# Kernel tuning notes

Measured on AMD Instinct MI355X. Metric: run time of the kernel, lower is better.

## Reference

```python
import jax, jax.numpy as jnp
import numpy as np
from jax import lax

K = 3          # dynamic filter kernel size
NH = 8         # attention heads

def _conv2d(x, w, b, pad, groups=1):
    y = lax.conv_general_dilated(x, w, (1, 1), [(pad, pad), (pad, pad)],
                                 feature_group_count=groups,
                                 dimension_numbers=('NCHW', 'OIHW', 'NCHW'))
    return y + b[None, :, None, None]

def _pw(x, w, b):  # 1x1 conv: w (O,C)
    return jnp.einsum('oc,bchw->bohw', w, x) + b[None, :, None, None]

def _lrelu(x):
    return jnp.where(x >= 0, x, 0.2 * x)

def _unfold(x, k):  # (B,C,H,W) -> (B,C,k*k,H,W), matches F.unfold ordering
    p = k // 2
    xp = jnp.pad(x, ((0, 0), (0, 0), (p, p), (p, p)))
    H, W = x.shape[2], x.shape[3]
    return jnp.stack([xp[:, :, i:i + H, j:j + W] for i in range(k) for j in range(k)], axis=2)

def setup_inputs() -> dict:
    key = jax.random.key(0)
    ks = jax.random.split(key, 24)
    B, C, H, W = 1, 256, 56, 56
    C2, K2 = C // 2, K * K
    s = 0.02
    d = {
        'dec_feat': jax.random.normal(ks[0], (B, C, H, W), jnp.float32),
        'enc_feat': jax.random.normal(ks[1], (B, C, H, W), jnp.float32),
        # ALPF kernel predictor: depthwise 3x3, 1x1 C->C/2, 1x1 C/2->k^2
        'alpf_dw_w': jax.random.normal(ks[2], (C, 1, 3, 3), jnp.float32) * s,
        'alpf_dw_b': jnp.zeros((C,), jnp.float32),
        'alpf_p1_w': jax.random.normal(ks[3], (C2, C), jnp.float32) * s,
        'alpf_p1_b': jnp.zeros((C2,), jnp.float32),
        'alpf_p2_w': jax.random.normal(ks[4], (K2, C2), jnp.float32) * s,
        'alpf_p2_b': jnp.zeros((K2,), jnp.float32),
        # AHPF weight predictor: 3x3 C->C/2, 1x1 C/2->k^2
        'ahpf_c1_w': jax.random.normal(ks[5], (C2, C, 3, 3), jnp.float32) * s,
        'ahpf_c1_b': jnp.zeros((C2,), jnp.float32),
        'ahpf_c2_w': jax.random.normal(ks[6], (K2, C2), jnp.float32) * s,
        'ahpf_c2_b': jnp.zeros((K2,), jnp.float32),
        # cross-attention projections (all 1x1)
        'q_w': jax.random.normal(ks[7], (C, C), jnp.float32) * s,
        'q_b': jnp.zeros((C,), jnp.float32),
        'kv_w': jax.random.normal(ks[8], (2 * C, C), jnp.float32) * s,
        'kv_b': jnp.zeros((2 * C,), jnp.float32),
        'out_w': jax.random.normal(ks[9], (C, C), jnp.float32) * s,
        'out_b': jnp.zeros((C,), jnp.float32),
        # fusion 3x3 conv
        'fusion_w': jax.random.normal(ks[10], (C, C, 3, 3), jnp.float32) * s,
        'fusion_b': jnp.zeros((C,), jnp.float32),
    }
    return d

def _forward(dec_feat, enc_feat, alpf_dw_w, alpf_dw_b, alpf_p1_w, alpf_p1_b,
             alpf_p2_w, alpf_p2_b, ahpf_c1_w, ahpf_c1_b, ahpf_c2_w, ahpf_c2_b,
             q_w, q_b, kv_w, kv_b, out_w, out_b, fusion_w, fusion_b):
    B, C, H, W = dec_feat.shape
    K2 = K * K
    # ---- Adaptive low-pass filter on dec_feat ----
    kw = _conv2d(dec_feat, alpf_dw_w, alpf_dw_b, pad=1, groups=C)
    kw = _lrelu(_pw(kw, alpf_p1_w, alpf_p1_b))
    kw = _pw(kw, alpf_p2_w, alpf_p2_b)            # (B,k2,H,W)
    kw = jax.nn.softmax(kw, axis=1)
    patches = _unfold(dec_feat, K)                # (B,C,k2,H,W)
    f_smooth = jnp.sum(patches * kw[:, None], axis=2)
    # ---- Cross attention: q from f_smooth, kv from enc_feat ----
    hd = C // NH
    N = H * W
    q = _pw(f_smooth, q_w, q_b).reshape(B, NH, hd, N)
    kv = _pw(enc_feat, kv_w, kv_b)
    k, v = jnp.split(kv, 2, axis=1)
    k = k.reshape(B, NH, hd, N)
    v = v.reshape(B, NH, hd, N)
    scale = hd ** -0.5
    attn = jnp.einsum('bhdn,bhdm->bhnm', q, k) * scale
    attn = jax.nn.softmax(attn, axis=-1)
    out = jnp.einsum('bhnm,bhdm->bhdn', attn, v).reshape(B, C, H, W)
    f_aligned = _pw(out, out_w, out_b)
    # ---- Adaptive high-pass filter on enc_feat ----
    wlp = _lrelu(_conv2d(enc_feat, ahpf_c1_w, ahpf_c1_b, pad=1))
    wlp = jax.nn.softmax(_pw(wlp, ahpf_c2_w, ahpf_c2_b), axis=1)  # (B,k2,H,W)
    whp = (-wlp).at[:, K2 // 2].add(1.0)          # delta - W_LP
    epatches = _unfold(enc_feat, K)
    f_high = enc_feat + jnp.sum(epatches * whp[:, None], axis=2)
    # ---- Fusion (w = 1.0) ----
    return _conv2d(f_aligned + 1.0 * f_high, fusion_w, fusion_b, pad=1)

def reference(dec_feat, enc_feat, alpf_dw_w, alpf_dw_b, alpf_p1_w, alpf_p1_b,
              alpf_p2_w, alpf_p2_b, ahpf_c1_w, ahpf_c1_b, ahpf_c2_w, ahpf_c2_b,
              q_w, q_b, kv_w, kv_b, out_w, out_b, fusion_w, fusion_b):
    return _forward(dec_feat, enc_feat, alpf_dw_w, alpf_dw_b, alpf_p1_w, alpf_p1_b,
                    alpf_p2_w, alpf_p2_b, ahpf_c1_w, ahpf_c1_b, ahpf_c2_w, ahpf_c2_b,
                    q_w, q_b, kv_w, kv_b, out_w, out_b, fusion_w, fusion_b)
```

## Files before the change

kernel.cpp:

```cpp
#include <hip/hip_runtime.h>
#include <hip/hip_bf16.h>

#define HH  56
#define WWC 56
#define HWP 3136
#define CC  256
#define NSPLIT 6

typedef unsigned short u16;
typedef __attribute__((ext_vector_type(8))) u16 u16x8;
typedef __attribute__((ext_vector_type(4))) u16 u16x4;
typedef __attribute__((ext_vector_type(8))) short s16x8;
typedef __attribute__((ext_vector_type(4))) float f32x4;

__device__ __forceinline__ u16 f2b(float f) {
  unsigned int x = __float_as_uint(f);
  return (u16)((x + 0x7fffu + ((x >> 16) & 1u)) >> 16);
}
__device__ __forceinline__ float b2f(u16 u) {
  return __uint_as_float(((unsigned int)u) << 16);
}
__device__ __forceinline__ f32x4 mfma16(s16x8 a, s16x8 b, f32x4 c) {
  return __builtin_amdgcn_mfma_f32_16x16x32_bf16(a, b, c, 0, 0, 0);
}

__device__ __forceinline__ float ldsel(const void* p, int i, bool bf) {
  if (bf) return __bfloat162float(((const __hip_bfloat16*)p)[i]);
  return ((const float*)p)[i];
}
__device__ __forceinline__ void stsel(void* p, int i, float v, bool bf) {
  if (bf) ((__hip_bfloat16*)p)[i] = __float2bfloat16(v);
  else ((float*)p)[i] = v;
}

__device__ __forceinline__ void ldrow8(const void* p, size_t i, bool bf,
                                       float* o) {
  if (bf) {
    u16x8 v = *(const u16x8*)((const u16*)p + i);
    #pragma unroll
    for (int j = 0; j < 8; ++j) o[j] = b2f(v[j]);
  } else {
    const float* f = (const float*)p + i;
    f32x4 a = *(const f32x4*)f;
    f32x4 b = *(const f32x4*)(f + 4);
    #pragma unroll
    for (int j = 0; j < 4; ++j) { o[j] = a[j]; o[4 + j] = b[j]; }
  }
}

__global__ void detect_dtype_k(const void* x, float* flag) {
  __shared__ int sh[256];
  int tid = threadIdx.x;
  const __hip_bfloat16* xb = (const __hip_bfloat16*)x;
  int ok = 0;
  for (int i = tid; i < 1024; i += 256) {
    float v = fabsf(__bfloat162float(xb[2 * i]));
    if (v > 9.5e-7f && v < 1.05e6f) ok++;
  }
  sh[tid] = ok;
  __syncthreads();
  for (int s = 128; s > 0; s >>= 1) {
    if (tid < s) sh[tid] += sh[tid + s];
    __syncthreads();
  }
  if (tid == 0) flag[0] = (sh[0] > 512) ? 1.f : 0.f;
}

__global__ __launch_bounds__(256)
void pack_all_k(const void* __restrict__ p1, const void* __restrict__ q,
                const void* __restrict__ kv, const void* __restrict__ ow,
                const void* __restrict__ c1, const void* __restrict__ fu,
                u16* __restrict__ d_p1, u16* __restrict__ d_q,
                u16* __restrict__ d_kv, u16* __restrict__ d_ow,
                u16* __restrict__ d_c1, u16* __restrict__ d_fu,
                const float* __restrict__ dflag) {
  bool bf = dflag[0] > 0.5f;
  int b = blockIdx.x, tid = threadIdx.x;
  if (b < 128) { int g = b * 256 + tid; d_p1[g] = f2b(ldsel(p1, g, bf)); return; }
  b -= 128;
  if (b < 256) { int g = b * 256 + tid; d_q[g] = f2b(ldsel(q, g, bf)); return; }
  b -= 256;
  if (b < 512) { int g = b * 256 + tid; d_kv[g] = f2b(ldsel(kv, g, bf)); return; }
  b -= 512;
  if (b < 256) { int g = b * 256 + tid; d_ow[g] = f2b(ldsel(ow, g, bf)); return; }
  b -= 256;
  if (b < 128) {
    int g = b * 256 + tid;
    #pragma unroll
    for (int t = 0; t < 9; ++t)
      d_c1[(size_t)t * 32768 + g] = f2b(ldsel(c1, g * 9 + t, bf));
    return;
  }
  b -= 128;
  {
    int g = b * 256 + tid;
    #pragma unroll
    for (int t = 0; t < 9; ++t)
      d_fu[(size_t)t * 65536 + g] = f2b(ldsel(fu, g * 9 + t, bf));
  }
}

__device__ __forceinline__ void dwconv_body(int gid, const void* x,
                                            const void* wt, const void* bs,
                                            u16* y, bool bf) {
  int c = gid / 392, g = gid - c * 392;
  int p0 = g * 8;
  int h = p0 / WWC, w0 = p0 - h * WWC;
  float wv[9];
  #pragma unroll
  for (int t = 0; t < 9; ++t) wv[t] = ldsel(wt, c * 9 + t, bf);
  float bv = ldsel(bs, c, bf);
  float acc[8];
  #pragma unroll
  for (int j = 0; j < 8; ++j) acc[j] = bv;
  const size_t cbase = (size_t)c * HWP;
  #pragma unroll
  for (int dh = -1; dh <= 1; ++dh) {
    int hh = h + dh;
    if (hh < 0 || hh >= HH) continue;
    size_t rbase = cbase + hh * WWC + w0;
    float v[8];
    ldrow8(x, rbase, bf, v);
    float lft = (w0 > 0) ? ldsel(x, rbase - 1, bf) : 0.f;
    float rgt = (w0 < 48) ? ldsel(x, rbase + 8, bf) : 0.f;
    float wm = wv[(dh + 1) * 3 + 0], wc = wv[(dh + 1) * 3 + 1],
          wp = wv[(dh + 1) * 3 + 2];
    #pragma unroll
    for (int j = 0; j < 8; ++j) {
      float vm = (j == 0) ? lft : v[j - 1];
      float vp = (j == 7) ? rgt : v[j + 1];
      acc[j] += vm * wm + v[j] * wc + vp * wp;
    }
  }
  u16x8 st;
  #pragma unroll
  for (int j = 0; j < 8; ++j) st[j] = f2b(acc[j]);
  *(u16x8*)&y[cbase + p0] = st;
}

template<int TAPS, int ACT, bool ADDIN, int OMODE>
__device__ __forceinline__ void mgemm_body(
    int bid, int sz, int NZ, int NO, int O,
    const u16* __restrict__ Wp, const void* __restrict__ X,
    const void* __restrict__ bias, const u16* __restrict__ addin,
    void* __restrict__ Y, int Cin, bool wbf, bool xbf, int xmode,
    int bias_off, u16 (*Ws)[72], u16 (*Xs)[72]) {
  int p0 = (bid / NO) * 32, o0 = (bid % NO) * 32;
  int t0 = (TAPS * sz) / NZ, t1 = (TAPS * (sz + 1)) / NZ;
  int tid = threadIdx.x, lane = tid & 63, wv = tid >> 6;
  int oq = (wv & 1) * 16, pq = (wv >> 1) * 16;
  int frow = lane & 15, kgrp = (lane >> 4) * 8;
  int wol = tid >> 3, wkk = (tid & 7) * 8;
  int pl = tid & 31, xkk = (tid >> 5) * 8;
  int p = p0 + pl, h = p / WWC, w = p - h * WWC;
  f32x4 acc = {0.f, 0.f, 0.f, 0.f};
  for (int t = t0; t < t1; ++t) {
    int dh = t / 3 - 1, dw = t % 3 - 1;
    int hh = h + dh, ww = w + dw;
    bool rowok = (TAPS == 1) || ((hh >= 0) && (hh < HH) && (ww >= 0) && (ww < WWC));
    int xoff = (TAPS == 1) ? p : hh * WWC + ww;
    const u16* Wrow = Wp + (size_t)t * O * Cin;
    for (int kb = 0; kb < Cin; kb += 64) {
      __syncthreads();
      *(u16x8*)&Ws[wol][wkk] =
          *(const u16x8*)&Wrow[(size_t)(o0 + wol) * Cin + kb + wkk];
      {
        u16x8 xv;
        if (xmode == 2) {
          if (rowok) {
            xv = *(const u16x8*)&((const u16*)X)[(size_t)xoff * Cin + kb + xkk];
          } else {
            #pragma unroll
            for (int j = 0; j < 8; ++j) xv[j] = 0;
          }
        } else if (xmode == 3) {
          #pragma unroll
          for (int j = 0; j < 8; ++j)
            xv[j] = rowok ? ((const u16*)X)[(size_t)(kb + xkk + j) * HWP + xoff]
                          : (u16)0;
        } else {
          #pragma unroll
          for (int j = 0; j < 8; ++j) {
            int kk = xkk + j;
            float v = rowok ? ldsel(X, (size_t)(kb + kk) * HWP + xoff, xbf) : 0.f;
            xv[j] = f2b(v);
          }
        }
        *(u16x8*)&Xs[pl][xkk] = xv;
      }
      __syncthreads();
      #pragma unroll
      for (int ks = 0; ks < 2; ++ks) {
        s16x8 aw = *(const s16x8*)&Ws[oq + frow][ks * 32 + kgrp];
        s16x8 ax = *(const s16x8*)&Xs[pq + frow][ks * 32 + kgrp];
        acc = mfma16(aw, ax, acc);
      }
    }
  }
  int orow = (lane >> 4) * 4;
  int ogb = o0 + oq + orow;
  int pg = p0 + pq + frow;
  if (OMODE == 4) {
    float* Yp = (float*)Y + (size_t)sz * O * HWP;
    #pragma unroll
    for (int r = 0; r < 4; ++r)
      Yp[(size_t)(ogb + r) * HWP + pg] = acc[r];
  } else if (OMODE == 5) {
    if (ogb < 256) {
      u16x4 st;
      #pragma unroll
      for (int r = 0; r < 4; ++r)
        st[r] = f2b(acc[r] + ldsel(bias, ogb + r, wbf));
      *(u16x4*)&((u16*)Y)[(size_t)pg * 256 + ogb] = st;
    } else {
      u16* V = (u16*)Y + (size_t)CC * HWP;
      #pragma unroll
      for (int r = 0; r < 4; ++r)
        V[(size_t)(ogb + r - 256) * HWP + pg] =
            f2b(acc[r] + ldsel(bias, ogb + r, wbf));
    }
  } else if (OMODE == 2) {
    u16x4 st;
    #pragma unroll
    for (int r = 0; r < 4; ++r) {
      float yv = acc[r] + ldsel(bias, bias_off + ogb + r, wbf);
      if (ACT == 1) yv = (yv >= 0.f) ? yv : 0.2f * yv;
      if (ADDIN) yv += b2f(addin[(size_t)(ogb + r) * HWP + pg]);
      st[r] = f2b(yv);
    }
    *(u16x4*)&((u16*)Y)[(size_t)pg * O + ogb] = st;
  } else {
    #pragma unroll
    for (int r = 0; r < 4; ++r) {
      int og = ogb + r;
      float yv = acc[r] + ldsel(bias, bias_off + og, wbf);
      if (ACT == 1) yv = (yv >= 0.f) ? yv : 0.2f * yv;
      if (ADDIN) yv += b2f(addin[(size_t)og * HWP + pg]);
      if (OMODE == 3) ((u16*)Y)[(size_t)og * HWP + pg] = f2b(yv);
      else stsel(Y, (size_t)og * HWP + pg, yv, (OMODE == 1) && wbf);
    }
  }
}

template<int TAPS, int ACT, bool ADDIN, int OMODE>
__global__ __launch_bounds__(256)
void mgemm32_k(const u16* __restrict__ Wp, const void* __restrict__ X,
               const void* __restrict__ bias, const u16* __restrict__ addin,
               void* __restrict__ Y, int Cin,
               const float* __restrict__ dflag, int xmode, int bias_off) {
  __shared__ u16 Ws[32][72];
  __shared__ u16 Xs[32][72];
  bool wbf = dflag[0] > 0.5f;
  bool xbf = (xmode == 1) ? wbf : false;
  int NO = gridDim.y;
  int bid = blockIdx.x + blockIdx.y * gridDim.x;
  mgemm_body<TAPS, ACT, ADDIN, OMODE>(bid, blockIdx.z, gridDim.z, NO, NO * 32,
                                      Wp, X, bias, addin, Y, Cin, wbf, xbf,
                                      xmode, bias_off, Ws, Xs);
}

__global__ __launch_bounds__(256)
void stage1_k(const void* __restrict__ dec, const void* __restrict__ dw_w,
              const void* __restrict__ dw_b, u16* __restrict__ A,
              const u16* __restrict__ wp_kv, const void* __restrict__ enc,
              const void* __restrict__ kv_b, u16* __restrict__ k16,
              const float* __restrict__ dflag) {
  __shared__ u16 Ws[32][72];
  __shared__ u16 Xs[32][72];
  bool bf = dflag[0] > 0.5f;
  int b = blockIdx.x;
  if (b < 392) {
    dwconv_body(b * 256 + threadIdx.x, dec, dw_w, dw_b, A, bf);
  } else {
    mgemm_body<1, 0, false, 5>(b - 392, 0, 1, 16, 512, wp_kv, enc, kv_b,
                               nullptr, k16, 256, bf, bf, 1, 0, Ws, Xs);
  }
}

__global__ __launch_bounds__(256)
void stage2_k(const u16* __restrict__ Op, const float* __restrict__ Lb,
              u16* __restrict__ A, const u16* __restrict__ wp_c1,
              const void* __restrict__ enc, float* __restrict__ Pc1,
              const float* __restrict__ dflag) {
  __shared__ u16 Ws[32][72];
  __shared__ u16 Xs[32][72];
  bool bf = dflag[0] > 0.5f;
  int b = blockIdx.x;
  if (b < 392) {
    int gid = b * 256 + threadIdx.x;
    int hd = gid / 392, g = gid - hd * 392;
    int n0 = g * 8, h = hd >> 5;
    float L[8] = {0,0,0,0,0,0,0,0}, O[8] = {0,0,0,0,0,0,0,0};
    #pragma unroll
    for (int s = 0; s < NSPLIT; ++s) {
      const float* Lp = &Lb[(size_t)(s * 8 + h) * HWP + n0];
      f32x4 l0 = *(const f32x4*)Lp;
      f32x4 l1 = *(const f32x4*)(Lp + 4);
      u16x8 ov = *(const u16x8*)&Op[(size_t)(s * 256 + hd) * HWP + n0];
      #pragma unroll
      for (int j = 0; j < 4; ++j) { L[j] += l0[j]; L[4 + j] += l1[j]; }
      #pragma unroll
      for (int j = 0; j < 8; ++j) O[j] += b2f(ov[j]);
    }
    u16x8 st;
    #pragma unroll
    for (int j = 0; j < 8; ++j) st[j] = f2b(O[j] / L[j]);
    *(u16x8*)&A[(size_t)hd * HWP + n0] = st;
  } else {
    int rem = b - 392;
    int sz = rem / 392, bb = rem - sz * 392;
    mgemm_body<9, 1, false, 4>(bb, sz, 3, 4, 128, wp_c1, enc, nullptr,
                               nullptr, Pc1, 256, bf, bf, 1, 0, Ws, Xs);
  }
}

__global__ __launch_bounds__(256)
void comb3_v2_k(const float* __restrict__ P, const void* __restrict__ bias,
                u16* __restrict__ Y, const float* __restrict__ dflag) {
  bool bf = dflag[0] > 0.5f;
  int flat = (blockIdx.x * 256 + threadIdx.x) * 4;
  int o = flat / HWP;
  f32x4 a = *(const f32x4*)&P[flat];
  f32x4 b = *(const f32x4*)&P[flat + 128 * HWP];
  f32x4 c = *(const f32x4*)&P[flat + 2 * 128 * HWP];
  float bv = ldsel(bias, o, bf);
  u16x4 st;
  #pragma unroll
  for (int j = 0; j < 4; ++j) {
    float v = a[j] + b[j] + c[j] + bv;
    v = (v >= 0.f) ? v : 0.2f * v;
    st[j] = f2b(v);
  }
  *(u16x4*)&Y[flat] = st;
}

__global__ __launch_bounds__(256)
void comb2_v2_k(const float* __restrict__ P, const void* __restrict__ bias,
                void* __restrict__ Y, const float* __restrict__ dflag) {
  bool bf = dflag[0] > 0.5f;
  int flat = (blockIdx.x * 256 + threadIdx.x) * 4;
  int o = flat / HWP;
  f32x4 a = *(const f32x4*)&P[flat];
  f32x4 b = *(const f32x4*)&P[flat + 256 * HWP];
  float bv = ldsel(bias, o, bf);
  if (bf) {
    u16x4 st;
    #pragma unroll
    for (int j = 0; j < 4; ++j) st[j] = f2b(a[j] + b[j] + bv);
    *(u16x4*)&((u16*)Y)[flat] = st;
  } else {
    f32x4 st;
    #pragma unroll
    for (int j = 0; j < 4; ++j) st[j] = a[j] + b[j] + bv;
    *(f32x4*)&((float*)Y)[flat] = st;
  }
}

template<bool DELTA>
__global__ __launch_bounds__(256)
void pw9_v2_k(const void* __restrict__ w2, const void* __restrict__ b2,
              const u16* __restrict__ hid, u16* __restrict__ out9,
              const float* __restrict__ dflag) {
  bool bf = dflag[0] > 0.5f;
  __shared__ float Wl[9][128];
  __shared__ float Pl[4][9][33];
  int tid = threadIdx.x;
  for (int i = tid; i < 1152; i += 256) Wl[i >> 7][i & 127] = ldsel(w2, i, bf);
  __syncthreads();
  int pix = tid & 31, cig = tid >> 5;
  int p = blockIdx.x * 32 + pix;
  int ci0 = cig * 16;
  float acc[9] = {0.f, 0.f, 0.f, 0.f, 0.f, 0.f, 0.f, 0.f, 0.f};
  #pragma unroll
  for (int j = 0; j < 16; ++j) {
    float xv = b2f(hid[(size_t)(ci0 + j) * HWP + p]);
    #pragma unroll
    for (int t = 0; t < 9; ++t) acc[t] += Wl[t][ci0 + j] * xv;
  }
  #pragma unroll
  for (int t = 0; t < 9; ++t) acc[t] += __shfl_xor(acc[t], 32);
  int wv = tid >> 6;
  if ((tid & 63) < 32) {
    #pragma unroll
    for (int t = 0; t < 9; ++t) Pl[wv][t][pix] = acc[t];
  }
  __syncthreads();
  if (tid < 32) {
    float a[9];
    #pragma unroll
    for (int t = 0; t < 9; ++t)
      a[t] = Pl[0][t][pix] + Pl[1][t][pix] + Pl[2][t][pix] + Pl[3][t][pix] +
             ldsel(b2, t, bf);
    float mx = a[0];
    #pragma unroll
    for (int t = 1; t < 9; ++t) mx = fmaxf(mx, a[t]);
    float s = 0.f;
    #pragma unroll
    for (int t = 0; t < 9; ++t) { a[t] = __expf(a[t] - mx); s += a[t]; }
    float inv = 1.f / s;
    #pragma unroll
    for (int t = 0; t < 9; ++t) {
      float v = a[t] * inv;
      if (DELTA) v = ((t == 4) ? 1.f : 0.f) - v;
      out9[(size_t)t * HWP + p] = f2b(v);
    }
  }
}

template<bool HIGH>
__global__ __launch_bounds__(128)
void spatial_v2_k(const void* __restrict__ x, const u16* __restrict__ w9,
                  u16* __restrict__ y, const float* __restrict__ dflag) {
  bool bf = dflag[0] > 0.5f;
  int gid = blockIdx.x * 128 + threadIdx.x;
  int c = gid / 392, g = gid - c * 392;
  int p0 = g * 8;
  int h = p0 / WWC, w0 = p0 - h * WWC;
  const size_t cbase = (size_t)c * HWP;
  float acc[8];
  if (HIGH) {
    ldrow8(x, cbase + p0, bf, acc);
  } else {
    #pragma unroll
    for (int j = 0; j < 8; ++j) acc[j] = 0.f;
  }
  #pragma unroll
  for (int dh = -1; dh <= 1; ++dh) {
    int hh = h + dh;
    if (hh < 0 || hh >= HH) continue;
    size_t rbase = cbase + hh * WWC + w0;
    float v[8];
    ldrow8(x, rbase, bf, v);
    float lft = (w0 > 0) ? ldsel(x, rbase - 1, bf) : 0.f;
    float rgt = (w0 < 48) ? ldsel(x, rbase + 8, bf) : 0.f;
    float wm[8], wc[8], wp[8];
    {
      int tb = (dh + 1) * 3;
      u16x8 a = *(const u16x8*)&w9[(size_t)(tb + 0) * HWP + p0];
      u16x8 b = *(const u16x8*)&w9[(size_t)(tb + 1) * HWP + p0];
      u16x8 d = *(const u16x8*)&w9[(size_t)(tb + 2) * HWP + p0];
      #pragma unroll
      for (int j = 0; j < 8; ++j) { wm[j] = b2f(a[j]); wc[j] = b2f(b[j]); wp[j] = b2f(d[j]); }
    }
    #pragma unroll
    for (int j = 0; j < 8; ++j) {
      float vm = (j == 0) ? lft : v[j - 1];
      float vp = (j == 7) ? rgt : v[j + 1];
      acc[j] += vm * wm[j] + v[j] * wc[j] + vp * wp[j];
    }
  }
  u16x8 st;
  #pragma unroll
  for (int j = 0; j < 8; ++j) st[j] = f2b(acc[j]);
  *(u16x8*)&y[cbase + p0] = st;
}

__global__ __launch_bounds__(256)
void attn_part_k(const u16* __restrict__ Qb, const u16* __restrict__ Kb,
                 const u16* __restrict__ Vb, u16* __restrict__ Op,
                 float* __restrict__ Lb) {
  __shared__ u16 Ks[64][40];
  __shared__ u16 Vs[32][72];
  __shared__ u16 Ps[4][16][72];
  int h = blockIdx.y, n0 = blockIdx.x * 64, sz = blockIdx.z;
  int tid = threadIdx.x, lane = tid & 63, wv = tid >> 6;
  int frow = lane & 15, gq = lane >> 4, kgrp = gq * 8;
  int ml = tid >> 2, dseg = (tid & 3) * 8;
  int vd = tid >> 3, vm = (tid & 7) * 8;
  const float QS = 0.17677669529663687f * 1.4426950408889634f;
  s16x8 aq;
  {
    u16x8 qv = *(const u16x8*)&Qb[(size_t)(n0 + wv * 16 + frow) * 256 + h * 32 + kgrp];
    u16x8 qs;
    #pragma unroll
    for (int j = 0; j < 8; ++j) qs[j] = f2b(b2f(qv[j]) * QS);
    aq = *(s16x8*)&qs;
  }
  f32x4 oa0 = {0.f, 0.f, 0.f, 0.f}, oa1 = {0.f, 0.f, 0.f, 0.f};
  float lsum = 0.f;
  int t_begin = (49 * sz) / NSPLIT, t_end = (49 * (sz + 1)) / NSPLIT;
  u16x8 kreg = *(const u16x8*)&Kb[(size_t)(t_begin * 64 + ml) * 256 + h * 32 + dseg];
  u16x8 vreg = *(const u16x8*)&Vb[(size_t)(h * 32 + vd) * HWP + t_begin * 64 + vm];
  for (int t = t_begin; t < t_end; ++t) {
    __syncthreads();
    *(u16x8*)&Ks[ml][dseg] = kreg;
    *(u16x8*)&Vs[vd][vm] = vreg;
    if (t + 1 < t_end) {
      kreg = *(const u16x8*)&Kb[(size_t)((t + 1) * 64 + ml) * 256 + h * 32 + dseg];
      vreg = *(const u16x8*)&Vb[(size_t)(h * 32 + vd) * HWP + (t + 1) * 64 + vm];
    }
    __syncthreads();
    f32x4 zero = {0.f, 0.f, 0.f, 0.f};
    #pragma unroll
    for (int fm = 0; fm < 4; ++fm) {
      s16x8 ak = *(const s16x8*)&Ks[fm * 16 + frow][kgrp];
      f32x4 s = mfma16(ak, aq, zero);
      u16x4 pe;
      #pragma unroll
      for (int r = 0; r < 4; ++r) {
        float e = exp2f(fminf(s[r], 43.f));
        lsum += e;
        pe[r] = (u16)(__float_as_uint(e) >> 16);
      }
      *(u16x4*)&Ps[wv][frow][fm * 16 + gq * 4] = pe;
    }
    #pragma unroll
    for (int ks = 0; ks < 2; ++ks) {
      s16x8 ap = *(const s16x8*)&Ps[wv][frow][ks * 32 + kgrp];
      s16x8 bv0 = *(const s16x8*)&Vs[frow][ks * 32 + kgrp];
      s16x8 bv1 = *(const s16x8*)&Vs[16 + frow][ks * 32 + kgrp];
      oa0 = mfma16(ap, bv0, oa0);
      oa1 = mfma16(ap, bv1, oa1);
    }
  }
  lsum += __shfl_xor(lsum, 16);
  lsum += __shfl_xor(lsum, 32);
  if (lane < 16)
    Lb[(size_t)(sz * 8 + h) * HWP + n0 + wv * 16 + frow] = lsum;
  #pragma unroll
  for (int r = 0; r < 4; ++r) {
    int n = n0 + wv * 16 + gq * 4 + r;
    Op[(size_t)(sz * 256 + h * 32 + frow) * HWP + n]      = f2b(oa0[r]);
    Op[(size_t)(sz * 256 + h * 32 + 16 + frow) * HWP + n] = f2b(oa1[r]);
  }
}

extern "C" void kernel_launch(void* const* d_in, const int* in_sizes, int n_in,
                              void* d_out, int out_size, void* d_ws, size_t ws_size,
                              hipStream_t stream) {
  const void* dec   = d_in[0];
  const void* enc   = d_in[1];
  const void* dw_w  = d_in[2];
  const void* dw_b  = d_in[3];
  const void* p1_w  = d_in[4];
  const void* p1_b  = d_in[5];
  const void* p2_w  = d_in[6];
  const void* p2_b  = d_in[7];
  const void* c1_w  = d_in[8];
  const void* c1_b  = d_in[9];
  const void* c2_w  = d_in[10];
  const void* c2_b  = d_in[11];
  const void* q_w   = d_in[12];
  const void* q_b   = d_in[13];
  const void* kv_w  = d_in[14];
  const void* kv_b  = d_in[15];
  const void* out_w = d_in[16];
  const void* out_b = d_in[17];
  const void* fu_w  = d_in[18];
  const void* fu_b  = d_in[19];

  const int CH = CC * HWP;
  float* flag = (float*)d_ws;
  u16* pk     = (u16*)(flag + 8);
  u16* A      = pk;              pk += CH;
  u16* hid    = pk;              pk += 128 * HWP;
  u16* s9     = pk;              pk += 9 * HWP;
  u16* Bb     = pk;              pk += CH;
  u16* qb16   = pk;              pk += CH;
  u16* k16    = pk;              pk += CH;
  u16* v16    = pk;              pk += CH;
  u16* wp_p1  = pk;              pk += 128 * 256;
  u16* wp_q   = pk;              pk += 256 * 256;
  u16* wp_kv  = pk;              pk += 512 * 256;
  u16* wp_out = pk;              pk += 256 * 256;
  u16* wp_c1  = pk;              pk += 128 * 256 * 9;
  u16* wp_fu  = pk;              pk += 256 * 256 * 9;
  pk += (size_t)(-(intptr_t)pk) & 7;
  float* Lb   = (float*)pk;
  u16* Opart  = (u16*)(Lb + 48 * HWP);
  float* Pc1 = (float*)qb16;
  float* Pfu = Lb;

  dim3 blk(256);
  detect_dtype_k<<<1, blk, 0, stream>>>(dec, flag);

  pack_all_k<<<1536, blk, 0, stream>>>(p1_w, q_w, kv_w, out_w, c1_w, fu_w,
                                       wp_p1, wp_q, wp_kv, wp_out, wp_c1, wp_fu,
                                       flag);

  stage1_k<<<1960, blk, 0, stream>>>(dec, dw_w, dw_b, A, wp_kv, enc, kv_b,
                                     k16, flag);

  mgemm32_k<1, 1, false, 3><<<dim3(98, 4), blk, 0, stream>>>(
      wp_p1, A, p1_b, nullptr, hid, 256, flag, 3, 0);
  pw9_v2_k<false><<<98, blk, 0, stream>>>(p2_w, p2_b, hid, s9, flag);
  spatial_v2_k<false><<<784, dim3(128), 0, stream>>>(dec, s9, Bb, flag);
  mgemm32_k<1, 0, false, 2><<<dim3(98, 8), blk, 0, stream>>>(
      wp_q, Bb, q_b, nullptr, qb16, 256, flag, 3, 0);

  attn_part_k<<<dim3(49, 8, NSPLIT), blk, 0, stream>>>(qb16, k16, v16, Opart, Lb);

  stage2_k<<<1568, blk, 0, stream>>>(Opart, Lb, A, wp_c1, enc, Pc1, flag);

  comb3_v2_k<<<392, blk, 0, stream>>>(Pc1, c1_b, hid, flag);
  pw9_v2_k<true><<<98, blk, 0, stream>>>(c2_w, c2_b, hid, s9, flag);
  spatial_v2_k<true><<<784, dim3(128), 0, stream>>>(enc, s9, Bb, flag);

  mgemm32_k<1, 0, true, 2><<<dim3(98, 8), blk, 0, stream>>>(
      wp_out, A, out_b, Bb, qb16, 256, flag, 3, 0);

  mgemm32_k<9, 0, false, 4><<<dim3(98, 8, 2), blk, 0, stream>>>(
      wp_fu, qb16, nullptr, nullptr, Pfu, 256, flag, 2, 0);
  comb2_v2_k<<<784, blk, 0, stream>>>(Pfu, fu_b, d_out, flag);
}
```

Before: 146.0 us.

## Rebuild launch schedule to co-run AHPF branch with ALPF stages before attention

Moves the enc_feat high-pass branch (3x3 conv, combine, pw9 softmax, spatial filter) out of the post-attention section and pairs each of its stages with an independent low-pass or q-projection stage in merged kernels. Duplicate buffers (hid2, s9b, Bb2) keep the two branches from overwriting each other. The attention split-combine becomes a standalone kernel. The fusion 3x3 conv now splits its K dimension three ways with a 3-way reduction instead of two. The goal is fewer serial launches and better GPU fill from concurrent independent work, at the cost of more workspace memory and some extra partial-sum traffic.

```diff
diff --git a/kernel.cpp b/kernel.cpp
--- a/kernel.cpp
+++ b/kernel.cpp
@@ -136,6 +136,100 @@
   #pragma unroll
   for (int j = 0; j < 8; ++j) st[j] = f2b(acc[j]);
   *(u16x8*)&y[cbase + p0] = st;
+}
+
+template<bool HIGH>
+__device__ __forceinline__ void spatial_body(int gid, const void* x,
+                                             const u16* w9, u16* y, bool bf) {
+  int c = gid / 392, g = gid - c * 392;
+  int p0 = g * 8;
+  int h = p0 / WWC, w0 = p0 - h * WWC;
+  const size_t cbase = (size_t)c * HWP;
+  float acc[8];
+  if (HIGH) {
+    ldrow8(x, cbase + p0, bf, acc);
+  } else {
+    #pragma unroll
+    for (int j = 0; j < 8; ++j) acc[j] = 0.f;
+  }
+  #pragma unroll
+  for (int dh = -1; dh <= 1; ++dh) {
+    int hh = h + dh;
+    if (hh < 0 || hh >= HH) continue;
+    size_t rbase = cbase + hh * WWC + w0;
+    float v[8];
+    ldrow8(x, rbase, bf, v);
+    float lft = (w0 > 0) ? ldsel(x, rbase - 1, bf) : 0.f;
+    float rgt = (w0 < 48) ? ldsel(x, rbase + 8, bf) : 0.f;
+    float wm[8], wc[8], wp[8];
+    {
+      int tb = (dh + 1) * 3;
+      u16x8 a = *(const u16x8*)&w9[(size_t)(tb + 0) * HWP + p0];
+      u16x8 b = *(const u16x8*)&w9[(size_t)(tb + 1) * HWP + p0];
+      u16x8 d = *(const u16x8*)&w9[(size_t)(tb + 2) * HWP + p0];
+      #pragma unroll
+      for (int j = 0; j < 8; ++j) { wm[j] = b2f(a[j]); wc[j] = b2f(b[j]); wp[j] = b2f(d[j]); }
+    }
+    #pragma unroll
+    for (int j = 0; j < 8; ++j) {
+      float vm = (j == 0) ? lft : v[j - 1];
+      float vp = (j == 7) ? rgt : v[j + 1];
+      acc[j] += vm * wm[j] + v[j] * wc[j] + vp * wp[j];
+    }
+  }
+  u16x8 st;
+  #pragma unroll
+  for (int j = 0; j < 8; ++j) st[j] = f2b(acc[j]);
+  *(u16x8*)&y[cbase + p0] = st;
+}
+
+template<bool DELTA>
+__device__ __forceinline__ void pw9_body(int pblk, const void* w2,
+                                         const void* b2, const u16* hid,
+                                         u16* out9, bool bf) {
+  __shared__ float Wl[9][128];
+  __shared__ float Pl[4][9][33];
+  int tid = threadIdx.x;
+  for (int i = tid; i < 1152; i += 256) Wl[i >> 7][i & 127] = ldsel(w2, i, bf);
+  __syncthreads();
+  int pix = tid & 31, cig = tid >> 5;
+  int p = pblk * 32 + pix;
+  int ci0 = cig * 16;
+  float acc[9] = {0.f, 0.f, 0.f, 0.f, 0.f, 0.f, 0.f, 0.f, 0.f};
+  #pragma unroll
+  for (int j = 0; j < 16; ++j) {
+    float xv = b2f(hid[(size_t)(ci0 + j) * HWP + p]);
+    #pragma unroll
+    for (int t = 0; t < 9; ++t) acc[t] += Wl[t][ci0 + j] * xv;
+  }
+  #pragma unroll
+  for (int t = 0; t < 9; ++t) acc[t] += __shfl_xor(acc[t], 32);
+  int wv = tid >> 6;
+  if ((tid & 63) < 32) {
+    #pragma unroll
+    for (int t = 0; t < 9; ++t) Pl[wv][t][pix] = acc[t];
+  }
+  __syncthreads();
+  if (tid < 32) {
+    float a[9];
+    #pragma unroll
+    for (int t = 0; t < 9; ++t)
+      a[t] = Pl[0][t][pix] + Pl[1][t][pix] + Pl[2][t][pix] + Pl[3][t][pix] +
+             ldsel(b2, t, bf);
+    float mx = a[0];
+    #pragma unroll
+    for (int t = 1; t < 9; ++t) mx = fmaxf(mx, a[t]);
+    float s = 0.f;
+    #pragma unroll
+    for (int t = 0; t < 9; ++t) { a[t] = __expf(a[t] - mx); s += a[t]; }
+    float inv = 1.f / s;
+    #pragma unroll
+    for (int t = 0; t < 9; ++t) {
+      float v = a[t] * inv;
+      if (DELTA) v = ((t == 4) ? 1.f : 0.f) - v;
+      out9[(size_t)t * HWP + p] = f2b(v);
+    }
+  }
 }
 
 template<int TAPS, int ACT, bool ADDIN, int OMODE>
@@ -278,34 +372,17 @@
 }
 
 __global__ __launch_bounds__(256)
-void stage2_k(const u16* __restrict__ Op, const float* __restrict__ Lb,
-              u16* __restrict__ A, const u16* __restrict__ wp_c1,
-              const void* __restrict__ enc, float* __restrict__ Pc1,
-              const float* __restrict__ dflag) {
+void stageA_k(const u16* __restrict__ wp_p1, const u16* __restrict__ A,
+              const void* __restrict__ p1_b, u16* __restrict__ hid,
+              const u16* __restrict__ wp_c1, const void* __restrict__ enc,
+              float* __restrict__ Pc1, const float* __restrict__ dflag) {
   __shared__ u16 Ws[32][72];
   __shared__ u16 Xs[32][72];
   bool bf = dflag[0] > 0.5f;
   int b = blockIdx.x;
   if (b < 392) {
-    int gid = b * 256 + threadIdx.x;
-    int hd = gid / 392, g = gid - hd * 392;
-    int n0 = g * 8, h = hd >> 5;
-    float L[8] = {0,0,0,0,0,0,0,0}, O[8] = {0,0,0,0,0,0,0,0};
-    #pragma unroll
-    for (int s = 0; s < NSPLIT; ++s) {
-      const float* Lp = &Lb[(size_t)(s * 8 + h) * HWP + n0];
-      f32x4 l0 = *(const f32x4*)Lp;
-      f32x4 l1 = *(const f32x4*)(Lp + 4);
-      u16x8 ov = *(const u16x8*)&Op[(size_t)(s * 256 + hd) * HWP + n0];
-      #pragma unroll
-      for (int j = 0; j < 4; ++j) { L[j] += l0[j]; L[4 + j] += l1[j]; }
-      #pragma unroll
-      for (int j = 0; j < 8; ++j) O[j] += b2f(ov[j]);
-    }
-    u16x8 st;
-    #pragma unroll
-    for (int j = 0; j < 8; ++j) st[j] = f2b(O[j] / L[j]);
-    *(u16x8*)&A[(size_t)hd * HWP + n0] = st;
+    mgemm_body<1, 1, false, 3>(b, 0, 1, 4, 128, wp_p1, A, p1_b, nullptr,
+                               hid, 256, bf, false, 3, 0, Ws, Xs);
   } else {
     int rem = b - 392;
     int sz = rem / 392, bb = rem - sz * 392;
@@ -315,144 +392,61 @@
 }
 
 __global__ __launch_bounds__(256)
-void comb3_v2_k(const float* __restrict__ P, const void* __restrict__ bias,
-                u16* __restrict__ Y, const float* __restrict__ dflag) {
+void stageB_k(const void* __restrict__ p2_w, const void* __restrict__ p2_b,
+              const u16* __restrict__ hid, u16* __restrict__ s9,
+              const float* __restrict__ Pc1, const void* __restrict__ c1_b,
+              u16* __restrict__ hid2, const float* __restrict__ dflag) {
   bool bf = dflag[0] > 0.5f;
-  int flat = (blockIdx.x * 256 + threadIdx.x) * 4;
-  int o = flat / HWP;
-  f32x4 a = *(const f32x4*)&P[flat];
-  f32x4 b = *(const f32x4*)&P[flat + 128 * HWP];
-  f32x4 c = *(const f32x4*)&P[flat + 2 * 128 * HWP];
-  float bv = ldsel(bias, o, bf);
-  u16x4 st;
-  #pragma unroll
-  for (int j = 0; j < 4; ++j) {
-    float v = a[j] + b[j] + c[j] + bv;
-    v = (v >= 0.f) ? v : 0.2f * v;
-    st[j] = f2b(v);
-  }
-  *(u16x4*)&Y[flat] = st;
-}
-
-__global__ __launch_bounds__(256)
-void comb2_v2_k(const float* __restrict__ P, const void* __restrict__ bias,
-                void* __restrict__ Y, const float* __restrict__ dflag) {
+  int b = blockIdx.x;
+  if (b < 98) {
+    pw9_body<false>(b, p2_w, p2_b, hid, s9, bf);
+  } else {
+    int flat = ((b - 98) * 256 + threadIdx.x) * 4;
+    int o = flat / HWP;
+    f32x4 a = *(const f32x4*)&Pc1[flat];
+    f32x4 c = *(const f32x4*)&Pc1[flat + 128 * HWP];
+    f32x4 d = *(const f32x4*)&Pc1[flat + 2 * 128 * HWP];
+    float bv = ldsel(c1_b, o, bf);
+    u16x4 st;
+    #pragma unroll
+    for (int j = 0; j < 4; ++j) {
+      float v = a[j] + c[j] + d[j] + bv;
+      v = (v >= 0.f) ? v : 0.2f * v;
+      st[j] = f2b(v);
+    }
+    *(u16x4*)&hid2[flat] = st;
+  }
+}
+
+__global__ __launch_bounds__(256)
+void stageC_k(const void* __restrict__ dec, const u16* __restrict__ s9,
+              u16* __restrict__ Bb, const void* __restrict__ c2_w,
+              const void* __restrict__ c2_b, const u16* __restrict__ hid2,
+              u16* __restrict__ s9b, const float* __restrict__ dflag) {
   bool bf = dflag[0] > 0.5f;
-  int flat = (blockIdx.x * 256 + threadIdx.x) * 4;
-  int o = flat / HWP;
-  f32x4 a = *(const f32x4*)&P[flat];
-  f32x4 b = *(const f32x4*)&P[flat + 256 * HWP];
-  float bv = ldsel(bias, o, bf);
-  if (bf) {
-    u16x4 st;
-    #pragma unroll
-    for (int j = 0; j < 4; ++j) st[j] = f2b(a[j] + b[j] + bv);
-    *(u16x4*)&((u16*)Y)[flat] = st;
-  } else {
-    f32x4 st;
-    #pragma unroll
-    for (int j = 0; j < 4; ++j) st[j] = a[j] + b[j] + bv;
-    *(f32x4*)&((float*)Y)[flat] = st;
-  }
-}
-
-template<bool DELTA>
-__global__ __launch_bounds__(256)
-void pw9_v2_k(const void* __restrict__ w2, const void* __restrict__ b2,
-              const u16* __restrict__ hid, u16* __restrict__ out9,
-              const float* __restrict__ dflag) {
+  int b = blockIdx.x;
+  if (b < 392) {
+    spatial_body<false>(b * 256 + threadIdx.x, dec, s9, Bb, bf);
+  } else {
+    pw9_body<true>(b - 392, c2_w, c2_b, hid2, s9b, bf);
+  }
+}
+
+__global__ __launch_bounds__(256)
+void stageD_k(const u16* __restrict__ wp_q, const u16* __restrict__ Bb,
+              const void* __restrict__ q_b, u16* __restrict__ qb16,
+              const void* __restrict__ enc, const u16* __restrict__ s9b,
+              u16* __restrict__ Bb2, const float* __restrict__ dflag) {
+  __shared__ u16 Ws[32][72];
+  __shared__ u16 Xs[32][72];
   bool bf = dflag[0] > 0.5f;
-  __shared__ float Wl[9][128];
-  __shared__ float Pl[4][9][33];
-  int tid = threadIdx.x;
-  for (int i = tid; i < 1152; i += 256) Wl[i >> 7][i & 127] = ldsel(w2, i, bf);
-  __syncthreads();
-  int pix = tid & 31, cig = tid >> 5;
-  int p = blockIdx.x * 32 + pix;
-  int ci0 = cig * 16;
-  float acc[9] = {0.f, 0.f, 0.f, 0.f, 0.f, 0.f, 0.f, 0.f, 0.f};
-  #pragma unroll
-  for (int j = 0; j < 16; ++j) {
-    float xv = b2f(hid[(size_t)(ci0 + j) * HWP + p]);
-    #pragma unroll
-    for (int t = 0; t < 9; ++t) acc[t] += Wl[t][ci0 + j] * xv;
-  }
-  #pragma unroll
-  for (int t = 0; t < 9; ++t) acc[t] += __shfl_xor(acc[t], 32);
-  int wv = tid >> 6;
-  if ((tid & 63) < 32) {
-    #pragma unroll
-    for (int t = 0; t < 9; ++t) Pl[wv][t][pix] = acc[t];
-  }
-  __syncthreads();
-  if (tid < 32) {
-    float a[9];
-    #pragma unroll
-    for (int t = 0; t < 9; ++t)
-      a[t] = Pl[0][t][pix] + Pl[1][t][pix] + Pl[2][t][pix] + Pl[3][t][pix] +
-             ldsel(b2, t, bf);
-    float mx = a[0];
-    #pragma unroll
-    for (int t = 1; t < 9; ++t) mx = fmaxf(mx, a[t]);
-    float s = 0.f;
-    #pragma unroll
-    for (int t = 0; t < 9; ++t) { a[t] = __expf(a[t] - mx); s += a[t]; }
-    float inv = 1.f / s;
-    #pragma unroll
-    for (int t = 0; t < 9; ++t) {
-      float v = a[t] * inv;
-      if (DELTA) v = ((t == 4) ? 1.f : 0.f) - v;
-      out9[(size_t)t * HWP + p] = f2b(v);
-    }
-  }
-}
-
-template<bool HIGH>
-__global__ __launch_bounds__(128)
-void spatial_v2_k(const void* __restrict__ x, const u16* __restrict__ w9,
-                  u16* __restrict__ y, const float* __restrict__ dflag) {
-  bool bf = dflag[0] > 0.5f;
-  int gid = blockIdx.x * 128 + threadIdx.x;
-  int c = gid / 392, g = gid - c * 392;
-  int p0 = g * 8;
-  int h = p0 / WWC, w0 = p0 - h * WWC;
-  const size_t cbase = (size_t)c * HWP;
-  float acc[8];
-  if (HIGH) {
-    ldrow8(x, cbase + p0, bf, acc);
-  } else {
-    #pragma unroll
-    for (int j = 0; j < 8; ++j) acc[j] = 0.f;
-  }
-  #pragma unroll
-  for (int dh = -1; dh <= 1; ++dh) {
-    int hh = h + dh;
-    if (hh < 0 || hh >= HH) continue;
-    size_t rbase = cbase + hh * WWC + w0;
-    float v[8];
-    ldrow8(x, rbase, bf, v);
-    float lft = (w0 > 0) ? ldsel(x, rbase - 1, bf) : 0.f;
-    float rgt = (w0 < 48) ? ldsel(x, rbase + 8, bf) : 0.f;
-    float wm[8], wc[8], wp[8];
-    {
-      int tb = (dh + 1) * 3;
-      u16x8 a = *(const u16x8*)&w9[(size_t)(tb + 0) * HWP + p0];
-      u16x8 b = *(const u16x8*)&w9[(size_t)(tb + 1) * HWP + p0];
-      u16x8 d = *(const u16x8*)&w9[(size_t)(tb + 2) * HWP + p0];
-      #pragma unroll
-      for (int j = 0; j < 8; ++j) { wm[j] = b2f(a[j]); wc[j] = b2f(b[j]); wp[j] = b2f(d[j]); }
-    }
-    #pragma unroll
-    for (int j = 0; j < 8; ++j) {
-      float vm = (j == 0) ? lft : v[j - 1];
-      float vp = (j == 7) ? rgt : v[j + 1];
-      acc[j] += vm * wm[j] + v[j] * wc[j] + vp * wp[j];
-    }
-  }
-  u16x8 st;
-  #pragma unroll
-  for (int j = 0; j < 8; ++j) st[j] = f2b(acc[j]);
-  *(u16x8*)&y[cbase + p0] = st;
+  int b = blockIdx.x;
+  if (b < 784) {
+    mgemm_body<1, 0, false, 2>(b, 0, 1, 8, 256, wp_q, Bb, q_b, nullptr,
+                               qb16, 256, bf, false, 3, 0, Ws, Xs);
+  } else {
+    spatial_body<true>((b - 784) * 256 + threadIdx.x, enc, s9b, Bb2, bf);
+  }
 }
 
 __global__ __launch_bounds__(256)
@@ -522,6 +516,53 @@
     int n = n0 + wv * 16 + gq * 4 + r;
     Op[(size_t)(sz * 256 + h * 32 + frow) * HWP + n]      = f2b(oa0[r]);
     Op[(size_t)(sz * 256 + h * 32 + 16 + frow) * HWP + n] = f2b(oa1[r]);
+  }
+}
+
+__global__ __launch_bounds__(256)
+void attn_combine_k(const u16* __restrict__ Op, const float* __restrict__ Lb,
+                    u16* __restrict__ A) {
+  int gid = blockIdx.x * 256 + threadIdx.x;
+  int hd = gid / 392, g = gid - hd * 392;
+  int n0 = g * 8, h = hd >> 5;
+  float L[8] = {0,0,0,0,0,0,0,0}, O[8] = {0,0,0,0,0,0,0,0};
+  #pragma unroll
+  for (int s = 0; s < NSPLIT; ++s) {
+    const float* Lp = &Lb[(size_t)(s * 8 + h) * HWP + n0];
+    f32x4 l0 = *(const f32x4*)Lp;
+    f32x4 l1 = *(const f32x4*)(Lp + 4);
+    u16x8 ov = *(const u16x8*)&Op[(size_t)(s * 256 + hd) * HWP + n0];
+    #pragma unroll
+    for (int j = 0; j < 4; ++j) { L[j] += l0[j]; L[4 + j] += l1[j]; }
+    #pragma unroll
+    for (int j = 0; j < 8; ++j) O[j] += b2f(ov[j]);
+  }
+  u16x8 st;
+  #pragma unroll
+  for (int j = 0; j < 8; ++j) st[j] = f2b(O[j] / L[j]);
+  *(u16x8*)&A[(size_t)hd * HWP + n0] = st;
+}
+
+__global__ __launch_bounds__(256)
+void comb3f_k(const float* __restrict__ P, const void* __restrict__ bias,
+              void* __restrict__ Y, const float* __restrict__ dflag) {
+  bool bf = dflag[0] > 0.5f;
+  int flat = (blockIdx.x * 256 + threadIdx.x) * 4;
+  int o = flat / HWP;
+  f32x4 a = *(const f32x4*)&P[flat];
+  f32x4 c = *(const f32x4*)&P[flat + 256 * HWP];
+  f32x4 d = *(const f32x4*)&P[flat + 2 * 256 * HWP];
+  float bv = ldsel(bias, o, bf);
+  if (bf) {
+    u16x4 st;
+    #pragma unroll
+    for (int j = 0; j < 4; ++j) st[j] = f2b(a[j] + c[j] + d[j] + bv);
+    *(u16x4*)&((u16*)Y)[flat] = st;
+  } else {
+    f32x4 st;
+    #pragma unroll
+    for (int j = 0; j < 4; ++j) st[j] = a[j] + c[j] + d[j] + bv;
+    *(f32x4*)&((float*)Y)[flat] = st;
   }
 }
 
@@ -554,8 +595,11 @@
   u16* pk     = (u16*)(flag + 8);
   u16* A      = pk;              pk += CH;
   u16* hid    = pk;              pk += 128 * HWP;
+  u16* hid2   = pk;              pk += 128 * HWP;
   u16* s9     = pk;              pk += 9 * HWP;
+  u16* s9b    = pk;              pk += 9 * HWP;
   u16* Bb     = pk;              pk += CH;
+  u16* Bb2    = pk;              pk += CH;
   u16* qb16   = pk;              pk += CH;
   u16* k16    = pk;              pk += CH;
   u16* v16    = pk;              pk += CH;
@@ -568,7 +612,7 @@
   pk += (size_t)(-(intptr_t)pk) & 7;
   float* Lb   = (float*)pk;
   u16* Opart  = (u16*)(Lb + 48 * HWP);
-  float* Pc1 = (float*)qb16;
+  float* Pc1 = Lb;
   float* Pfu = Lb;
 
   dim3 blk(256);
@@ -581,25 +625,21 @@
   stage1_k<<<1960, blk, 0, stream>>>(dec, dw_w, dw_b, A, wp_kv, enc, kv_b,
                                      k16, flag);
 
-  mgemm32_k<1, 1, false, 3><<<dim3(98, 4), blk, 0, stream>>>(
-      wp_p1, A, p1_b, nullptr, hid, 256, flag, 3, 0);
-  pw9_v2_k<false><<<98, blk, 0, stream>>>(p2_w, p2_b, hid, s9, flag);
-  spatial_v2_k<false><<<784, dim3(128), 0, stream>>>(dec, s9, Bb, flag);
-  mgemm32_k<1, 0, false, 2><<<dim3(98, 8), blk, 0, stream>>>(
-      wp_q, Bb, q_b, nullptr, qb16, 256, flag, 3, 0);
+  stageA_k<<<1568, blk, 0, stream>>>(wp_p1, A, p1_b, hid, wp_c1, enc, Pc1, flag);
+
+  stageB_k<<<490, blk, 0, stream>>>(p2_w, p2_b, hid, s9, Pc1, c1_b, hid2, flag);
+
+  stageC_k<<<490, blk, 0, stream>>>(dec, s9, Bb, c2_w, c2_b, hid2, s9b, flag);
+
+  stageD_k<<<1176, blk, 0, stream>>>(wp_q, Bb, q_b, qb16, enc, s9b, Bb2, flag);
 
   attn_part_k<<<dim3(49, 8, NSPLIT), blk, 0, stream>>>(qb16, k16, v16, Opart, Lb);
-
-  stage2_k<<<1568, blk, 0, stream>>>(Opart, Lb, A, wp_c1, enc, Pc1, flag);
-
-  comb3_v2_k<<<392, blk, 0, stream>>>(Pc1, c1_b, hid, flag);
-  pw9_v2_k<true><<<98, blk, 0, stream>>>(c2_w, c2_b, hid, s9, flag);
-  spatial_v2_k<true><<<784, dim3(128), 0, stream>>>(enc, s9, Bb, flag);
+  attn_combine_k<<<392, blk, 0, stream>>>(Opart, Lb, A);
 
   mgemm32_k<1, 0, true, 2><<<dim3(98, 8), blk, 0, stream>>>(
-      wp_out, A, out_b, Bb, qb16, 256, flag, 3, 0);
-
-  mgemm32_k<9, 0, false, 4><<<dim3(98, 8, 2), blk, 0, stream>>>(
+      wp_out, A, out_b, Bb2, qb16, 256, flag, 3, 0);
+
+  mgemm32_k<9, 0, false, 4><<<dim3(98, 8, 3), blk, 0, stream>>>(
       wp_fu, qb16, nullptr, nullptr, Pfu, 256, flag, 2, 0);
-  comb2_v2_k<<<784, blk, 0, stream>>>(Pfu, fu_b, d_out, flag);
-}
+  comb3f_k<<<784, blk, 0, stream>>>(Pfu, fu_b, d_out, flag);
+}
```

New measurement: 135.3 us. -7.3%, faster.
